# Kernel optimization log

Measured on AMD Instinct MI355X. Metric: run time of the kernel, lower is better.

Reference implementation:

```python
import jax, jax.numpy as jnp
import numpy as np

B, T = 2, 2048
D_MODEL, D_HIDDEN = 1024, 2048
N_EXPERTS, TOP_K = 8, 2
N_TOKENS = B * T
CAPACITY = 2 * N_TOKENS * TOP_K // N_EXPERTS  # 4096


def setup_inputs() -> dict:
    key = jax.random.key(0)
    k_x, k_rw, k_w, k_v, k_o = jax.random.split(key, 5)
    x = jax.random.normal(k_x, (B, T, D_MODEL), jnp.float32)
    # router: nn.Linear(d_model, n_experts) -> weight [E, D], bias [E]
    router_w = jax.random.normal(k_rw, (N_EXPERTS, D_MODEL), jnp.float32) * D_MODEL ** -0.5
    router_b = jnp.zeros((N_EXPERTS,), jnp.float32)
    # stacked expert params, matching SwiGLU init scales
    W = jax.random.normal(k_w, (N_EXPERTS, D_MODEL, D_HIDDEN), jnp.float32) * D_MODEL ** -0.5
    V = jax.random.normal(k_v, (N_EXPERTS, D_MODEL, D_HIDDEN), jnp.float32) * D_MODEL ** -0.5
    W_out = jax.random.normal(k_o, (N_EXPERTS, D_HIDDEN, D_MODEL), jnp.float32) * D_HIDDEN ** -0.5
    return {"x": x, "router_w": router_w, "router_b": router_b, "W": W, "V": V, "W_out": W_out}


def reference(x, router_w, router_b, W, V, W_out):
    Bq, Tq, D = x.shape
    N = Bq * Tq
    x_flat = x.reshape(N, D)

    # token-level top-k routing
    router_logits = x_flat @ router_w.T + router_b            # [N, E]
    top_vals, top_ids = jax.lax.top_k(router_logits, TOP_K)   # [N, K]
    top_probs = jax.nn.softmax(top_vals, axis=-1)             # [N, K]

    # pad row N: gathers with fill index N read zeros / contribute zero weight
    x_pad = jnp.concatenate([x_flat, jnp.zeros((1, D), x_flat.dtype)], axis=0)
    probs_pad = jnp.concatenate([top_probs, jnp.zeros((1, TOP_K), top_probs.dtype)], axis=0)

    out = jnp.zeros((N + 1, D), x_flat.dtype)
    for e in range(N_EXPERTS):  # static small loop over experts
        tok, slot = jnp.nonzero(top_ids == e, size=CAPACITY, fill_value=(N, 0))
        w = probs_pad[tok, slot][:, None]     # [C, 1], zero for padding slots
        xin = x_pad[tok]                      # [C, D] gather
        a = xin @ W[e]                        # [C, H]
        b = xin @ V[e]                        # [C, H]
        y = (a * (b * jax.nn.sigmoid(b))) @ W_out[e]  # SwiGLU: a * swish(b) -> [C, D]
        out = out.at[tok].add(y * w)          # weighted scatter-add
    return out[:N].reshape(Bq, Tq, D)
```

## Files before the change

### kernel.cpp

```cpp
#include <hip/hip_runtime.h>
#include <cstdint>
#include <cstddef>

#define N_TOK 4096
#define DM    1024
#define DH    2048
#define NE    8
#define NSLOT 8192

typedef short bf16x8_t __attribute__((ext_vector_type(8)));
typedef float f32x4    __attribute__((ext_vector_type(4)));
typedef unsigned short u16x8 __attribute__((ext_vector_type(8)));

__device__ __forceinline__ unsigned short f2bf(float f) {
  union { float f; unsigned int u; } v; v.f = f;
  unsigned int u = v.u;
  u += 0x7fffu + ((u >> 16) & 1u);
  return (unsigned short)(u >> 16);
}

__device__ __forceinline__ float bf2f(unsigned short h) {
  union { unsigned int u; float f; } v; v.u = ((unsigned int)h) << 16;
  return v.f;
}

#define GLD16(gp, lp)                                                          \
  __builtin_amdgcn_global_load_lds(                                            \
      (const __attribute__((address_space(1))) void*)(gp),                     \
      (__attribute__((address_space(3))) void*)(lp), 16, 0, 0)

__device__ __forceinline__ int expert_off(const int* __restrict__ counts, int e, int* cnt) {
  int off = 0, s = 0;
#pragma unroll
  for (int i = 0; i < NE; i++) { if (i == e) off = s; s += counts[i]; }
  *cnt = counts[e];
  return off;
}

__global__ __launch_bounds__(256) void k_transpose(
    const float* __restrict__ W, const float* __restrict__ V,
    const float* __restrict__ Wout, unsigned short* __restrict__ B1t,
    unsigned short* __restrict__ B2t, int* __restrict__ counts) {
  if (blockIdx.z == 0 && blockIdx.x == 0 && blockIdx.y == 0 && threadIdx.x < NE)
    counts[threadIdx.x] = 0;

  const int z = blockIdx.z;
  const float* s;
  unsigned short* d;
  int R, C, xt, yt;
  if (z < 16) {
    const int e = z & 7;
    s = ((z < 8) ? W : V) + (size_t)e * DM * DH;
    d = B1t + (size_t)e * 4096 * DM + (size_t)((z < 8) ? 0 : DH) * DM;
    R = DM; C = DH; xt = blockIdx.x; yt = blockIdx.y;
  } else {
    const int e = z - 16;
    s = Wout + (size_t)e * DH * DM;
    d = B2t + (size_t)e * DM * DH;
    R = DH; C = DM;
    const int flat = blockIdx.x * 16 + blockIdx.y;
    xt = flat & 15; yt = flat >> 4;
  }
  const int c0 = xt * 64, r0 = yt * 64;
  __shared__ float tile[64][65];
  const int t = threadIdx.x;
  {
    const int cc = (t & 15) * 4;
#pragma unroll
    for (int j = 0; j < 4; j++) {
      const int r = (t >> 4) + j * 16;
      const float4 v = *(const float4*)(s + (size_t)(r0 + r) * C + c0 + cc);
      tile[r][cc + 0] = v.x; tile[r][cc + 1] = v.y;
      tile[r][cc + 2] = v.z; tile[r][cc + 3] = v.w;
    }
  }
  __syncthreads();
  {
    const int r8 = (t & 7) * 8;
#pragma unroll
    for (int j = 0; j < 2; j++) {
      const int c = (t >> 3) + j * 32;
      u16x8 o;
#pragma unroll
      for (int i = 0; i < 8; i++) o[i] = f2bf(tile[r8 + i][c]);
      *(u16x8*)(d + (size_t)(c0 + c) * R + r0 + r8) = o;
    }
  }
}

__global__ __launch_bounds__(256) void k_router(
    const float* __restrict__ x, const float* __restrict__ rw,
    const float* __restrict__ rb, int* __restrict__ counts,
    int* __restrict__ meta_e, int* __restrict__ meta_idx,
    float* __restrict__ meta_p) {
  const int wv = threadIdx.x >> 6;
  const int l  = threadIdx.x & 63;
  const int tk = blockIdx.x * 4 + wv;
  const float* xr = x + (size_t)tk * DM;

  float acc[NE];
#pragma unroll
  for (int e = 0; e < NE; e++) acc[e] = 0.f;
#pragma unroll 4
  for (int i = 0; i < DM / 64; i++) {
    const float xv = xr[i * 64 + l];
#pragma unroll
    for (int e = 0; e < NE; e++) acc[e] += xv * rw[e * DM + i * 64 + l];
  }
#pragma unroll
  for (int off = 32; off > 0; off >>= 1) {
#pragma unroll
    for (int e = 0; e < NE; e++) acc[e] += __shfl_xor(acc[e], off);
  }
#pragma unroll
  for (int e = 0; e < NE; e++) acc[e] += rb[e];

  float v0 = -1e30f; int e0 = 0;
#pragma unroll
  for (int e = 0; e < NE; e++) { if (acc[e] > v0) { v0 = acc[e]; e0 = e; } }
  float v1 = -1e30f; int e1 = 0;
#pragma unroll
  for (int e = 0; e < NE; e++) { if (e != e0 && acc[e] > v1) { v1 = acc[e]; e1 = e; } }
  const float p0 = 1.0f / (1.0f + __expf(v1 - v0));
  const float p1 = 1.0f - p0;

  if (l == 0) {
    const int i0 = atomicAdd(&counts[e0], 1);
    const int i1 = atomicAdd(&counts[e1], 1);
    meta_e[tk * 2 + 0] = e0;  meta_e[tk * 2 + 1] = e1;
    meta_idx[tk * 2 + 0] = i0; meta_idx[tk * 2 + 1] = i1;
    meta_p[tk * 2 + 0] = p0;  meta_p[tk * 2 + 1] = p1;
  }
}

__global__ __launch_bounds__(256) void k_gather(
    const float* __restrict__ x, const int* __restrict__ meta_e,
    const int* __restrict__ meta_idx, const int* __restrict__ counts,
    unsigned short* __restrict__ Xg) {
  const int tk = blockIdx.x;
  int offs[NE];
  { int s = 0;
#pragma unroll
    for (int e = 0; e < NE; e++) { offs[e] = s; s += counts[e]; } }
  const int s0 = tk * 2, s1 = s0 + 1;
  const int g0 = offs[meta_e[s0]] + meta_idx[s0];
  const int g1 = offs[meta_e[s1]] + meta_idx[s1];
  const float4 v = ((const float4*)(x + (size_t)tk * DM))[threadIdx.x];
  ushort4 o;
  o.x = f2bf(v.x); o.y = f2bf(v.y); o.z = f2bf(v.z); o.w = f2bf(v.w);
  *(ushort4*)(Xg + (size_t)g0 * DM + threadIdx.x * 4) = o;
  *(ushort4*)(Xg + (size_t)g1 * DM + threadIdx.x * 4) = o;
}

__global__ __launch_bounds__(256, 2) void k_gemm1(
    const unsigned short* __restrict__ Xg, const unsigned short* __restrict__ B1t,
    unsigned short* __restrict__ G, const int* __restrict__ counts) {
  const int e = blockIdx.z;
  int cnt;
  const int off = expert_off(counts, e, &cnt);
  const int mt = blockIdx.y;
  if (mt * 128 >= cnt) return;
  const int h0 = blockIdx.x * 128;
  const int row_base = off + mt * 128;

  __shared__ unsigned short As[2][128 * 32];
  __shared__ unsigned short Ws[2][128 * 32];
  __shared__ unsigned short Vs[2][128 * 32];

  const int t = threadIdx.x;
  const int l = t & 63;
  const int w = t >> 6;
  const int wm = (w >> 1) * 64;
  const int wn = (w & 1) * 64;
  const int lr = l & 15;
  const int kq = (l >> 4) * 8;

  const unsigned short* Bw = B1t + ((size_t)e * 4096 + h0) * DM;
  const unsigned short* Bv = Bw + (size_t)DH * DM;

  const int c0 = t, c1 = t + 256;
  const int ar0 = c0 >> 2, ak0 = (c0 & 3) * 8;
  const int ar1 = c1 >> 2, ak1 = (c1 & 3) * 8;
  const int arow0 = min(row_base + ar0, NSLOT - 1);
  const int arow1 = min(row_base + ar1, NSLOT - 1);

  f32x4 acc_a[4][4], acc_b[4][4];
  const f32x4 z4 = {0.f, 0.f, 0.f, 0.f};
#pragma unroll
  for (int i = 0; i < 4; i++)
#pragma unroll
    for (int j = 0; j < 4; j++) { acc_a[i][j] = z4; acc_b[i][j] = z4; }

  for (int k0 = 0; k0 < DM; k0 += 64) {
    __syncthreads();
    GLD16(Xg + (size_t)arow0 * DM + k0 + ak0,      &As[0][c0 * 8]);
    GLD16(Xg + (size_t)arow1 * DM + k0 + ak1,      &As[0][c1 * 8]);
    GLD16(Xg + (size_t)arow0 * DM + k0 + 32 + ak0, &As[1][c0 * 8]);
    GLD16(Xg + (size_t)arow1 * DM + k0 + 32 + ak1, &As[1][c1 * 8]);
    GLD16(Bw + (size_t)ar0 * DM + k0 + ak0,        &Ws[0][c0 * 8]);
    GLD16(Bw + (size_t)ar1 * DM + k0 + ak1,        &Ws[0][c1 * 8]);
    GLD16(Bw + (size_t)ar0 * DM + k0 + 32 + ak0,   &Ws[1][c0 * 8]);
    GLD16(Bw + (size_t)ar1 * DM + k0 + 32 + ak1,   &Ws[1][c1 * 8]);
    GLD16(Bv + (size_t)ar0 * DM + k0 + ak0,        &Vs[0][c0 * 8]);
    GLD16(Bv + (size_t)ar1 * DM + k0 + ak1,        &Vs[0][c1 * 8]);
    GLD16(Bv + (size_t)ar0 * DM + k0 + 32 + ak0,   &Vs[1][c0 * 8]);
    GLD16(Bv + (size_t)ar1 * DM + k0 + 32 + ak1,   &Vs[1][c1 * 8]);
    __syncthreads();

#pragma unroll
    for (int ks = 0; ks < 2; ks++) {
      bf16x8_t af[4], wf[4], vf[4];
#pragma unroll
      for (int mi = 0; mi < 4; mi++)
        af[mi] = *(const bf16x8_t*)&As[ks][(wm + mi * 16 + lr) * 32 + kq];
#pragma unroll
      for (int ni = 0; ni < 4; ni++) {
        wf[ni] = *(const bf16x8_t*)&Ws[ks][(wn + ni * 16 + lr) * 32 + kq];
        vf[ni] = *(const bf16x8_t*)&Vs[ks][(wn + ni * 16 + lr) * 32 + kq];
      }
#pragma unroll
      for (int mi = 0; mi < 4; mi++)
#pragma unroll
        for (int ni = 0; ni < 4; ni++) {
          acc_a[mi][ni] = __builtin_amdgcn_mfma_f32_16x16x32_bf16(af[mi], wf[ni], acc_a[mi][ni], 0, 0, 0);
          acc_b[mi][ni] = __builtin_amdgcn_mfma_f32_16x16x32_bf16(af[mi], vf[ni], acc_b[mi][ni], 0, 0, 0);
        }
    }
  }

  const int q4 = (l >> 4) * 4;
#pragma unroll
  for (int mi = 0; mi < 4; mi++) {
#pragma unroll
    for (int r = 0; r < 4; r++) {
      const int mloc = mt * 128 + wm + mi * 16 + q4 + r;
      if (mloc >= cnt) continue;
      unsigned short* grow = G + (size_t)(off + mloc) * DH;
#pragma unroll
      for (int ni = 0; ni < 4; ni++) {
        const int h = h0 + wn + ni * 16 + lr;
        const float a = acc_a[mi][ni][r];
        const float b = acc_b[mi][ni][r];
        const float s = b / (1.0f + __expf(-b));
        grow[h] = f2bf(a * s);
      }
    }
  }
}

__global__ __launch_bounds__(256, 2) void k_gemm2(
    const unsigned short* __restrict__ G, const unsigned short* __restrict__ B2t,
    unsigned short* __restrict__ Y, const int* __restrict__ counts) {
  const int z = blockIdx.z;
  const int e = z & 7;
  const int half = z >> 3;
  int cnt;
  const int off = expert_off(counts, e, &cnt);
  const int mt = blockIdx.y;
  if (mt * 128 >= cnt) return;
  const int n0 = blockIdx.x * 128;
  const int row_base = off + mt * 128;
  const int kbase = half * 1024;

  __shared__ unsigned short As[2][128 * 32];
  __shared__ unsigned short Bs[2][128 * 32];

  const int t = threadIdx.x;
  const int l = t & 63;
  const int w = t >> 6;
  const int wm = (w >> 1) * 64;
  const int wn = (w & 1) * 64;
  const int lr = l & 15;
  const int kq = (l >> 4) * 8;

  const unsigned short* Bp = B2t + ((size_t)e * DM + n0) * DH;

  const int c0 = t, c1 = t + 256;
  const int ar0 = c0 >> 2, ak0 = (c0 & 3) * 8;
  const int ar1 = c1 >> 2, ak1 = (c1 & 3) * 8;
  const int arow0 = min(row_base + ar0, NSLOT - 1);
  const int arow1 = min(row_base + ar1, NSLOT - 1);

  f32x4 acc[4][4];
  const f32x4 z4 = {0.f, 0.f, 0.f, 0.f};
#pragma unroll
  for (int i = 0; i < 4; i++)
#pragma unroll
    for (int j = 0; j < 4; j++) acc[i][j] = z4;

  for (int kk = 0; kk < 1024; kk += 64) {
    const int k0 = kbase + kk;
    __syncthreads();
    GLD16(G + (size_t)arow0 * DH + k0 + ak0,      &As[0][c0 * 8]);
    GLD16(G + (size_t)arow1 * DH + k0 + ak1,      &As[0][c1 * 8]);
    GLD16(G + (size_t)arow0 * DH + k0 + 32 + ak0, &As[1][c0 * 8]);
    GLD16(G + (size_t)arow1 * DH + k0 + 32 + ak1, &As[1][c1 * 8]);
    GLD16(Bp + (size_t)ar0 * DH + k0 + ak0,       &Bs[0][c0 * 8]);
    GLD16(Bp + (size_t)ar1 * DH + k0 + ak1,       &Bs[0][c1 * 8]);
    GLD16(Bp + (size_t)ar0 * DH + k0 + 32 + ak0,  &Bs[1][c0 * 8]);
    GLD16(Bp + (size_t)ar1 * DH + k0 + 32 + ak1,  &Bs[1][c1 * 8]);
    __syncthreads();

#pragma unroll
    for (int ks = 0; ks < 2; ks++) {
      bf16x8_t af[4], bf[4];
#pragma unroll
      for (int mi = 0; mi < 4; mi++)
        af[mi] = *(const bf16x8_t*)&As[ks][(wm + mi * 16 + lr) * 32 + kq];
#pragma unroll
      for (int ni = 0; ni < 4; ni++)
        bf[ni] = *(const bf16x8_t*)&Bs[ks][(wn + ni * 16 + lr) * 32 + kq];
#pragma unroll
      for (int mi = 0; mi < 4; mi++)
#pragma unroll
        for (int ni = 0; ni < 4; ni++)
          acc[mi][ni] = __builtin_amdgcn_mfma_f32_16x16x32_bf16(af[mi], bf[ni], acc[mi][ni], 0, 0, 0);
    }
  }

  unsigned short* Yh = Y + (size_t)half * NSLOT * DM;
  const int q4 = (l >> 4) * 4;
#pragma unroll
  for (int mi = 0; mi < 4; mi++) {
#pragma unroll
    for (int r = 0; r < 4; r++) {
      const int mloc = mt * 128 + wm + mi * 16 + q4 + r;
      if (mloc >= cnt) continue;
      unsigned short* yrow = Yh + (size_t)(off + mloc) * DM;
#pragma unroll
      for (int ni = 0; ni < 4; ni++)
        yrow[n0 + wn + ni * 16 + lr] = f2bf(acc[mi][ni][r]);
    }
  }
}

__global__ __launch_bounds__(256) void k_combine(
    const unsigned short* __restrict__ Y, const int* __restrict__ meta_e,
    const int* __restrict__ meta_idx, const float* __restrict__ meta_p,
    const int* __restrict__ counts, float* __restrict__ out) {
  const int tk = blockIdx.x;
  int offs[NE];
  { int s = 0;
#pragma unroll
    for (int e = 0; e < NE; e++) { offs[e] = s; s += counts[e]; } }
  const int s0 = tk * 2, s1 = s0 + 1;
  const int g0 = offs[meta_e[s0]] + meta_idx[s0];
  const int g1 = offs[meta_e[s1]] + meta_idx[s1];
  const float w0 = meta_p[s0], w1 = meta_p[s1];
  const unsigned short* Y1 = Y + (size_t)NSLOT * DM;
  const ushort4 a0 = ((const ushort4*)(Y  + (size_t)g0 * DM))[threadIdx.x];
  const ushort4 a1 = ((const ushort4*)(Y1 + (size_t)g0 * DM))[threadIdx.x];
  const ushort4 b0 = ((const ushort4*)(Y  + (size_t)g1 * DM))[threadIdx.x];
  const ushort4 b1 = ((const ushort4*)(Y1 + (size_t)g1 * DM))[threadIdx.x];
  float4 o;
  o.x = w0 * (bf2f(a0.x) + bf2f(a1.x)) + w1 * (bf2f(b0.x) + bf2f(b1.x));
  o.y = w0 * (bf2f(a0.y) + bf2f(a1.y)) + w1 * (bf2f(b0.y) + bf2f(b1.y));
  o.z = w0 * (bf2f(a0.z) + bf2f(a1.z)) + w1 * (bf2f(b0.z) + bf2f(b1.z));
  o.w = w0 * (bf2f(a0.w) + bf2f(a1.w)) + w1 * (bf2f(b0.w) + bf2f(b1.w));
  ((float4*)(out + (size_t)tk * DM))[threadIdx.x] = o;
}

extern "C" void kernel_launch(void* const* d_in, const int* in_sizes, int n_in,
                              void* d_out, int out_size, void* d_ws, size_t ws_size,
                              hipStream_t stream) {
  const float* x    = (const float*)d_in[0];
  const float* rw   = (const float*)d_in[1];
  const float* rb   = (const float*)d_in[2];
  const float* W    = (const float*)d_in[3];
  const float* V    = (const float*)d_in[4];
  const float* Wout = (const float*)d_in[5];
  float* out = (float*)d_out;

  char* p = (char*)d_ws;
  unsigned short* B1t = (unsigned short*)p; p += (size_t)NE * 4096 * DM * 2;
  unsigned short* Y   = (unsigned short*)B1t;
  unsigned short* B2t = (unsigned short*)p; p += (size_t)NE * DM * DH * 2;
  unsigned short* Xg  = (unsigned short*)p; p += (size_t)NSLOT * DM * 2;
  unsigned short* G   = (unsigned short*)p; p += (size_t)NSLOT * DH * 2;
  int*   counts      = (int*)p;   p += 256;
  int*   meta_e      = (int*)p;   p += (size_t)N_TOK * 2 * 4;
  int*   meta_idx    = (int*)p;   p += (size_t)N_TOK * 2 * 4;
  float* meta_p      = (float*)p; p += (size_t)N_TOK * 2 * 4;

  k_transpose<<<dim3(32, 16, 24), 256, 0, stream>>>(W, V, Wout, B1t, B2t, counts);
  k_router<<<N_TOK / 4, 256, 0, stream>>>(x, rw, rb, counts, meta_e, meta_idx, meta_p);
  k_gather<<<N_TOK, 256, 0, stream>>>(x, meta_e, meta_idx, counts, Xg);
  k_gemm1<<<dim3(DH / 128, NSLOT / 128, NE), 256, 0, stream>>>(Xg, B1t, G, counts);
  k_gemm2<<<dim3(DM / 128, NSLOT / 128, 2 * NE), 256, 0, stream>>>(G, B2t, Y, counts);
  k_combine<<<N_TOK, 256, 0, stream>>>(Y, meta_e, meta_idx, meta_p, counts, out);
}
```

Measured before the change: 493.1 us.

## Pipeline expert GEMMs with 4-stage async LDS buffers, swizzle, 256-row tiles

Both expert GEMM kernels move to 512-thread blocks with 256-row M tiles and a 4-deep ring of LDS stages filled by global_load_lds. Loads for stage s+3 are issued before computing stage s, with explicit vmcnt waits and a single barrier per step instead of two full syncs per K chunk. An XOR swizzle is applied to the LDS layout to cut bank conflicts on fragment reads, and MFMA sections run at raised wave priority. LDS use grows considerably (about 160KB for gemm1), which may limit occupancy to one block per CU despite the launch bound, and larger M tiles waste more work on partially filled expert tiles.

```diff
diff --git a/kernel.cpp b/kernel.cpp
--- a/kernel.cpp
+++ b/kernel.cpp
@@ -28,6 +28,14 @@
   __builtin_amdgcn_global_load_lds(                                            \
       (const __attribute__((address_space(1))) void*)(gp),                     \
       (__attribute__((address_space(3))) void*)(lp), 16, 0, 0)
+
+#define WAITVM(N) asm volatile("s_waitcnt vmcnt(" #N ")" ::: "memory")
+#define BAR()                                                                  \
+  do {                                                                         \
+    __builtin_amdgcn_sched_barrier(0);                                         \
+    __builtin_amdgcn_s_barrier();                                              \
+    __builtin_amdgcn_sched_barrier(0);                                         \
+  } while (0)
 
 __device__ __forceinline__ int expert_off(const int* __restrict__ counts, int e, int* cnt) {
   int off = 0, s = 0;
@@ -152,20 +160,20 @@
   *(ushort4*)(Xg + (size_t)g1 * DM + threadIdx.x * 4) = o;
 }
 
-__global__ __launch_bounds__(256, 2) void k_gemm1(
+__global__ __launch_bounds__(512, 2) void k_gemm1(
     const unsigned short* __restrict__ Xg, const unsigned short* __restrict__ B1t,
     unsigned short* __restrict__ G, const int* __restrict__ counts) {
   const int e = blockIdx.z;
   int cnt;
   const int off = expert_off(counts, e, &cnt);
   const int mt = blockIdx.y;
-  if (mt * 128 >= cnt) return;
+  if (mt * 256 >= cnt) return;
   const int h0 = blockIdx.x * 128;
-  const int row_base = off + mt * 128;
-
-  __shared__ unsigned short As[2][128 * 32];
-  __shared__ unsigned short Ws[2][128 * 32];
-  __shared__ unsigned short Vs[2][128 * 32];
+  const int row_base = off + mt * 256;
+
+  __shared__ unsigned short As[4][256 * 32];
+  __shared__ unsigned short Ws[4][128 * 32];
+  __shared__ unsigned short Vs[4][128 * 32];
 
   const int t = threadIdx.x;
   const int l = t & 63;
@@ -178,11 +186,27 @@
   const unsigned short* Bw = B1t + ((size_t)e * 4096 + h0) * DM;
   const unsigned short* Bv = Bw + (size_t)DH * DM;
 
-  const int c0 = t, c1 = t + 256;
-  const int ar0 = c0 >> 2, ak0 = (c0 & 3) * 8;
-  const int ar1 = c1 >> 2, ak1 = (c1 & 3) * 8;
-  const int arow0 = min(row_base + ar0, NSLOT - 1);
-  const int arow1 = min(row_base + ar1, NSLOT - 1);
+  const int cA0 = t, cA1 = t + 512;
+  const int rA0 = cA0 >> 2, rA1 = cA1 >> 2;
+  const int kA0 = ((cA0 & 3) ^ ((rA0 >> 1) & 3)) << 3;
+  const int kA1 = ((cA1 & 3) ^ ((rA1 >> 1) & 3)) << 3;
+  const size_t aoff0 = (size_t)min(row_base + rA0, NSLOT - 1) * DM + kA0;
+  const size_t aoff1 = (size_t)min(row_base + rA1, NSLOT - 1) * DM + kA1;
+  const int rB = t >> 2;
+  const int kB = ((t & 3) ^ ((rB >> 1) & 3)) << 3;
+  const size_t boff = (size_t)rB * DM + kB;
+
+#define STAGE1(s)                                                              \
+  do {                                                                         \
+    const int k0_ = (s) * 32;                                                  \
+    unsigned short* As_ = As[(s) & 3];                                         \
+    unsigned short* Ws_ = Ws[(s) & 3];                                         \
+    unsigned short* Vs_ = Vs[(s) & 3];                                         \
+    GLD16(Xg + aoff0 + k0_, &As_[cA0 * 8]);                                    \
+    GLD16(Xg + aoff1 + k0_, &As_[cA1 * 8]);                                    \
+    GLD16(Bw + boff + k0_, &Ws_[t * 8]);                                       \
+    GLD16(Bv + boff + k0_, &Vs_[t * 8]);                                       \
+  } while (0)
 
   f32x4 acc_a[4][4], acc_b[4][4];
   const f32x4 z4 = {0.f, 0.f, 0.f, 0.f};
@@ -191,49 +215,52 @@
 #pragma unroll
     for (int j = 0; j < 4; j++) { acc_a[i][j] = z4; acc_b[i][j] = z4; }
 
-  for (int k0 = 0; k0 < DM; k0 += 64) {
-    __syncthreads();
-    GLD16(Xg + (size_t)arow0 * DM + k0 + ak0,      &As[0][c0 * 8]);
-    GLD16(Xg + (size_t)arow1 * DM + k0 + ak1,      &As[0][c1 * 8]);
-    GLD16(Xg + (size_t)arow0 * DM + k0 + 32 + ak0, &As[1][c0 * 8]);
-    GLD16(Xg + (size_t)arow1 * DM + k0 + 32 + ak1, &As[1][c1 * 8]);
-    GLD16(Bw + (size_t)ar0 * DM + k0 + ak0,        &Ws[0][c0 * 8]);
-    GLD16(Bw + (size_t)ar1 * DM + k0 + ak1,        &Ws[0][c1 * 8]);
-    GLD16(Bw + (size_t)ar0 * DM + k0 + 32 + ak0,   &Ws[1][c0 * 8]);
-    GLD16(Bw + (size_t)ar1 * DM + k0 + 32 + ak1,   &Ws[1][c1 * 8]);
-    GLD16(Bv + (size_t)ar0 * DM + k0 + ak0,        &Vs[0][c0 * 8]);
-    GLD16(Bv + (size_t)ar1 * DM + k0 + ak1,        &Vs[0][c1 * 8]);
-    GLD16(Bv + (size_t)ar0 * DM + k0 + 32 + ak0,   &Vs[1][c0 * 8]);
-    GLD16(Bv + (size_t)ar1 * DM + k0 + 32 + ak1,   &Vs[1][c1 * 8]);
-    __syncthreads();
-
-#pragma unroll
-    for (int ks = 0; ks < 2; ks++) {
-      bf16x8_t af[4], wf[4], vf[4];
-#pragma unroll
-      for (int mi = 0; mi < 4; mi++)
-        af[mi] = *(const bf16x8_t*)&As[ks][(wm + mi * 16 + lr) * 32 + kq];
+  STAGE1(0); STAGE1(1); STAGE1(2);
+  WAITVM(8);
+  BAR();
+
+  const int NS = DM / 32;
+#pragma unroll 2
+  for (int s = 0; s < NS; s++) {
+    if (s + 3 < NS) STAGE1(s + 3);
+    const unsigned short* Asl = As[s & 3];
+    const unsigned short* Wsl = Ws[s & 3];
+    const unsigned short* Vsl = Vs[s & 3];
+    bf16x8_t af[4], wf[4], vf[4];
+#pragma unroll
+    for (int mi = 0; mi < 4; mi++) {
+      const int row = wm + mi * 16 + lr;
+      af[mi] = *(const bf16x8_t*)&Asl[(row * 32 + kq) ^ (((row >> 1) & 3) << 3)];
+    }
+#pragma unroll
+    for (int ni = 0; ni < 4; ni++) {
+      const int row = wn + ni * 16 + lr;
+      const int idx = (row * 32 + kq) ^ (((row >> 1) & 3) << 3);
+      wf[ni] = *(const bf16x8_t*)&Wsl[idx];
+      vf[ni] = *(const bf16x8_t*)&Vsl[idx];
+    }
+    __builtin_amdgcn_s_setprio(1);
+#pragma unroll
+    for (int mi = 0; mi < 4; mi++)
 #pragma unroll
       for (int ni = 0; ni < 4; ni++) {
-        wf[ni] = *(const bf16x8_t*)&Ws[ks][(wn + ni * 16 + lr) * 32 + kq];
-        vf[ni] = *(const bf16x8_t*)&Vs[ks][(wn + ni * 16 + lr) * 32 + kq];
+        acc_a[mi][ni] = __builtin_amdgcn_mfma_f32_16x16x32_bf16(af[mi], wf[ni], acc_a[mi][ni], 0, 0, 0);
+        acc_b[mi][ni] = __builtin_amdgcn_mfma_f32_16x16x32_bf16(af[mi], vf[ni], acc_b[mi][ni], 0, 0, 0);
       }
-#pragma unroll
-      for (int mi = 0; mi < 4; mi++)
-#pragma unroll
-        for (int ni = 0; ni < 4; ni++) {
-          acc_a[mi][ni] = __builtin_amdgcn_mfma_f32_16x16x32_bf16(af[mi], wf[ni], acc_a[mi][ni], 0, 0, 0);
-          acc_b[mi][ni] = __builtin_amdgcn_mfma_f32_16x16x32_bf16(af[mi], vf[ni], acc_b[mi][ni], 0, 0, 0);
-        }
-    }
-  }
+    __builtin_amdgcn_s_setprio(0);
+    if (s < NS - 3)       { WAITVM(8); }
+    else if (s == NS - 3) { WAITVM(4); }
+    else if (s == NS - 2) { WAITVM(0); }
+    if (s < NS - 1) BAR();
+  }
+#undef STAGE1
 
   const int q4 = (l >> 4) * 4;
 #pragma unroll
   for (int mi = 0; mi < 4; mi++) {
 #pragma unroll
     for (int r = 0; r < 4; r++) {
-      const int mloc = mt * 128 + wm + mi * 16 + q4 + r;
+      const int mloc = mt * 256 + wm + mi * 16 + q4 + r;
       if (mloc >= cnt) continue;
       unsigned short* grow = G + (size_t)(off + mloc) * DH;
 #pragma unroll
@@ -241,14 +268,14 @@
         const int h = h0 + wn + ni * 16 + lr;
         const float a = acc_a[mi][ni][r];
         const float b = acc_b[mi][ni][r];
-        const float s = b / (1.0f + __expf(-b));
-        grow[h] = f2bf(a * s);
+        const float sgl = b / (1.0f + __expf(-b));
+        grow[h] = f2bf(a * sgl);
       }
     }
   }
 }
 
-__global__ __launch_bounds__(256, 2) void k_gemm2(
+__global__ __launch_bounds__(512, 2) void k_gemm2(
     const unsigned short* __restrict__ G, const unsigned short* __restrict__ B2t,
     unsigned short* __restrict__ Y, const int* __restrict__ counts) {
   const int z = blockIdx.z;
@@ -257,13 +284,13 @@
   int cnt;
   const int off = expert_off(counts, e, &cnt);
   const int mt = blockIdx.y;
-  if (mt * 128 >= cnt) return;
+  if (mt * 256 >= cnt) return;
   const int n0 = blockIdx.x * 128;
-  const int row_base = off + mt * 128;
+  const int row_base = off + mt * 256;
   const int kbase = half * 1024;
 
-  __shared__ unsigned short As[2][128 * 32];
-  __shared__ unsigned short Bs[2][128 * 32];
+  __shared__ unsigned short As[4][256 * 32];
+  __shared__ unsigned short Bs[4][128 * 32];
 
   const int t = threadIdx.x;
   const int l = t & 63;
@@ -275,11 +302,25 @@
 
   const unsigned short* Bp = B2t + ((size_t)e * DM + n0) * DH;
 
-  const int c0 = t, c1 = t + 256;
-  const int ar0 = c0 >> 2, ak0 = (c0 & 3) * 8;
-  const int ar1 = c1 >> 2, ak1 = (c1 & 3) * 8;
-  const int arow0 = min(row_base + ar0, NSLOT - 1);
-  const int arow1 = min(row_base + ar1, NSLOT - 1);
+  const int cA0 = t, cA1 = t + 512;
+  const int rA0 = cA0 >> 2, rA1 = cA1 >> 2;
+  const int kA0 = ((cA0 & 3) ^ ((rA0 >> 1) & 3)) << 3;
+  const int kA1 = ((cA1 & 3) ^ ((rA1 >> 1) & 3)) << 3;
+  const size_t aoff0 = (size_t)min(row_base + rA0, NSLOT - 1) * DH + kA0;
+  const size_t aoff1 = (size_t)min(row_base + rA1, NSLOT - 1) * DH + kA1;
+  const int rB = t >> 2;
+  const int kB = ((t & 3) ^ ((rB >> 1) & 3)) << 3;
+  const size_t boff = (size_t)rB * DH + kB;
+
+#define STAGE2(s)                                                              \
+  do {                                                                         \
+    const int k0_ = kbase + (s) * 32;                                          \
+    unsigned short* As_ = As[(s) & 3];                                         \
+    unsigned short* Bs_ = Bs[(s) & 3];                                         \
+    GLD16(G + aoff0 + k0_, &As_[cA0 * 8]);                                     \
+    GLD16(G + aoff1 + k0_, &As_[cA1 * 8]);                                     \
+    GLD16(Bp + boff + k0_, &Bs_[t * 8]);                                       \
+  } while (0)
 
   f32x4 acc[4][4];
   const f32x4 z4 = {0.f, 0.f, 0.f, 0.f};
@@ -288,35 +329,40 @@
 #pragma unroll
     for (int j = 0; j < 4; j++) acc[i][j] = z4;
 
-  for (int kk = 0; kk < 1024; kk += 64) {
-    const int k0 = kbase + kk;
-    __syncthreads();
-    GLD16(G + (size_t)arow0 * DH + k0 + ak0,      &As[0][c0 * 8]);
-    GLD16(G + (size_t)arow1 * DH + k0 + ak1,      &As[0][c1 * 8]);
-    GLD16(G + (size_t)arow0 * DH + k0 + 32 + ak0, &As[1][c0 * 8]);
-    GLD16(G + (size_t)arow1 * DH + k0 + 32 + ak1, &As[1][c1 * 8]);
-    GLD16(Bp + (size_t)ar0 * DH + k0 + ak0,       &Bs[0][c0 * 8]);
-    GLD16(Bp + (size_t)ar1 * DH + k0 + ak1,       &Bs[0][c1 * 8]);
-    GLD16(Bp + (size_t)ar0 * DH + k0 + 32 + ak0,  &Bs[1][c0 * 8]);
-    GLD16(Bp + (size_t)ar1 * DH + k0 + 32 + ak1,  &Bs[1][c1 * 8]);
-    __syncthreads();
-
-#pragma unroll
-    for (int ks = 0; ks < 2; ks++) {
-      bf16x8_t af[4], bf[4];
-#pragma unroll
-      for (int mi = 0; mi < 4; mi++)
-        af[mi] = *(const bf16x8_t*)&As[ks][(wm + mi * 16 + lr) * 32 + kq];
+  STAGE2(0); STAGE2(1); STAGE2(2);
+  WAITVM(6);
+  BAR();
+
+  const int NS = 1024 / 32;
+#pragma unroll 2
+  for (int s = 0; s < NS; s++) {
+    if (s + 3 < NS) STAGE2(s + 3);
+    const unsigned short* Asl = As[s & 3];
+    const unsigned short* Bsl = Bs[s & 3];
+    bf16x8_t af[4], bf[4];
+#pragma unroll
+    for (int mi = 0; mi < 4; mi++) {
+      const int row = wm + mi * 16 + lr;
+      af[mi] = *(const bf16x8_t*)&Asl[(row * 32 + kq) ^ (((row >> 1) & 3) << 3)];
+    }
+#pragma unroll
+    for (int ni = 0; ni < 4; ni++) {
+      const int row = wn + ni * 16 + lr;
+      bf[ni] = *(const bf16x8_t*)&Bsl[(row * 32 + kq) ^ (((row >> 1) & 3) << 3)];
+    }
+    __builtin_amdgcn_s_setprio(1);
+#pragma unroll
+    for (int mi = 0; mi < 4; mi++)
 #pragma unroll
       for (int ni = 0; ni < 4; ni++)
-        bf[ni] = *(const bf16x8_t*)&Bs[ks][(wn + ni * 16 + lr) * 32 + kq];
-#pragma unroll
-      for (int mi = 0; mi < 4; mi++)
-#pragma unroll
-        for (int ni = 0; ni < 4; ni++)
-          acc[mi][ni] = __builtin_amdgcn_mfma_f32_16x16x32_bf16(af[mi], bf[ni], acc[mi][ni], 0, 0, 0);
-    }
-  }
+        acc[mi][ni] = __builtin_amdgcn_mfma_f32_16x16x32_bf16(af[mi], bf[ni], acc[mi][ni], 0, 0, 0);
+    __builtin_amdgcn_s_setprio(0);
+    if (s < NS - 3)       { WAITVM(6); }
+    else if (s == NS - 3) { WAITVM(3); }
+    else if (s == NS - 2) { WAITVM(0); }
+    if (s < NS - 1) BAR();
+  }
+#undef STAGE2
 
   unsigned short* Yh = Y + (size_t)half * NSLOT * DM;
   const int q4 = (l >> 4) * 4;
@@ -324,7 +370,7 @@
   for (int mi = 0; mi < 4; mi++) {
 #pragma unroll
     for (int r = 0; r < 4; r++) {
-      const int mloc = mt * 128 + wm + mi * 16 + q4 + r;
+      const int mloc = mt * 256 + wm + mi * 16 + q4 + r;
       if (mloc >= cnt) continue;
       unsigned short* yrow = Yh + (size_t)(off + mloc) * DM;
 #pragma unroll
@@ -385,7 +431,7 @@
   k_transpose<<<dim3(32, 16, 24), 256, 0, stream>>>(W, V, Wout, B1t, B2t, counts);
   k_router<<<N_TOK / 4, 256, 0, stream>>>(x, rw, rb, counts, meta_e, meta_idx, meta_p);
   k_gather<<<N_TOK, 256, 0, stream>>>(x, meta_e, meta_idx, counts, Xg);
-  k_gemm1<<<dim3(DH / 128, NSLOT / 128, NE), 256, 0, stream>>>(Xg, B1t, G, counts);
-  k_gemm2<<<dim3(DM / 128, NSLOT / 128, 2 * NE), 256, 0, stream>>>(G, B2t, Y, counts);
+  k_gemm1<<<dim3(DH / 128, NSLOT / 256, NE), 512, 0, stream>>>(Xg, B1t, G, counts);
+  k_gemm2<<<dim3(DM / 128, NSLOT / 256, 2 * NE), 512, 0, stream>>>(G, B2t, Y, counts);
   k_combine<<<N_TOK, 256, 0, stream>>>(Y, meta_e, meta_idx, meta_p, counts, out);
 }
```

New measurement: 549.0 us. 11.3% more time.

## Double-buffer LDS tiles with prefetch and XOR-swizzle layout in both expert GEMMs

Applied to the files above, without the earlier changes.

Both grouped GEMM kernels now stage 32-wide K slices into two alternating LDS buffers, issuing the next slice's global-to-LDS loads before the MFMA work on the current slice. This replaces the old load-all-then-compute structure with its two barriers per 64-wide step. The K offset inside each 32-element row is also XOR-swizzled by row bits, applied consistently on store and read, to cut LDS bank conflicts on fragment reads. The cost is one barrier per 32-K step instead of per 64-K step, and it relies on GLD16 being asynchronous enough to overlap with compute.

```diff
diff --git a/kernel.cpp b/kernel.cpp
--- a/kernel.cpp
+++ b/kernel.cpp
@@ -179,10 +179,23 @@
   const unsigned short* Bv = Bw + (size_t)DH * DM;
 
   const int c0 = t, c1 = t + 256;
-  const int ar0 = c0 >> 2, ak0 = (c0 & 3) * 8;
-  const int ar1 = c1 >> 2, ak1 = (c1 & 3) * 8;
-  const int arow0 = min(row_base + ar0, NSLOT - 1);
-  const int arow1 = min(row_base + ar1, NSLOT - 1);
+  const int r0 = c0 >> 2, r1 = c1 >> 2;
+  const int k0s = ((c0 & 3) ^ ((r0 >> 1) & 3)) << 3;
+  const int k1s = ((c1 & 3) ^ ((r1 >> 1) & 3)) << 3;
+  const size_t aoff0 = (size_t)min(row_base + r0, NSLOT - 1) * DM + k0s;
+  const size_t aoff1 = (size_t)min(row_base + r1, NSLOT - 1) * DM + k1s;
+  const size_t boff0 = (size_t)r0 * DM + k0s;
+  const size_t boff1 = (size_t)r1 * DM + k1s;
+
+#define STG1(buf, kk)                                                          \
+  do {                                                                         \
+    GLD16(Xg + aoff0 + (kk), &As[buf][c0 * 8]);                                \
+    GLD16(Xg + aoff1 + (kk), &As[buf][c1 * 8]);                                \
+    GLD16(Bw + boff0 + (kk), &Ws[buf][c0 * 8]);                                \
+    GLD16(Bw + boff1 + (kk), &Ws[buf][c1 * 8]);                                \
+    GLD16(Bv + boff0 + (kk), &Vs[buf][c0 * 8]);                                \
+    GLD16(Bv + boff1 + (kk), &Vs[buf][c1 * 8]);                                \
+  } while (0)
 
   f32x4 acc_a[4][4], acc_b[4][4];
   const f32x4 z4 = {0.f, 0.f, 0.f, 0.f};
@@ -191,42 +204,36 @@
 #pragma unroll
     for (int j = 0; j < 4; j++) { acc_a[i][j] = z4; acc_b[i][j] = z4; }
 
-  for (int k0 = 0; k0 < DM; k0 += 64) {
+  STG1(0, 0);
+  __syncthreads();
+
+  const int NS = DM / 32;
+  for (int s = 0; s < NS; s++) {
+    const int cur = s & 1;
+    bf16x8_t af[4], wf[4], vf[4];
+#pragma unroll
+    for (int mi = 0; mi < 4; mi++) {
+      const int row = wm + mi * 16 + lr;
+      af[mi] = *(const bf16x8_t*)&As[cur][(row * 32 + kq) ^ (((row >> 1) & 3) << 3)];
+    }
+#pragma unroll
+    for (int ni = 0; ni < 4; ni++) {
+      const int row = wn + ni * 16 + lr;
+      const int idx = (row * 32 + kq) ^ (((row >> 1) & 3) << 3);
+      wf[ni] = *(const bf16x8_t*)&Ws[cur][idx];
+      vf[ni] = *(const bf16x8_t*)&Vs[cur][idx];
+    }
+    if (s + 1 < NS) STG1(cur ^ 1, (s + 1) * 32);
+#pragma unroll
+    for (int mi = 0; mi < 4; mi++)
+#pragma unroll
+      for (int ni = 0; ni < 4; ni++) {
+        acc_a[mi][ni] = __builtin_amdgcn_mfma_f32_16x16x32_bf16(af[mi], wf[ni], acc_a[mi][ni], 0, 0, 0);
+        acc_b[mi][ni] = __builtin_amdgcn_mfma_f32_16x16x32_bf16(af[mi], vf[ni], acc_b[mi][ni], 0, 0, 0);
+      }
     __syncthreads();
-    GLD16(Xg + (size_t)arow0 * DM + k0 + ak0,      &As[0][c0 * 8]);
-    GLD16(Xg + (size_t)arow1 * DM + k0 + ak1,      &As[0][c1 * 8]);
-    GLD16(Xg + (size_t)arow0 * DM + k0 + 32 + ak0, &As[1][c0 * 8]);
-    GLD16(Xg + (size_t)arow1 * DM + k0 + 32 + ak1, &As[1][c1 * 8]);
-    GLD16(Bw + (size_t)ar0 * DM + k0 + ak0,        &Ws[0][c0 * 8]);
-    GLD16(Bw + (size_t)ar1 * DM + k0 + ak1,        &Ws[0][c1 * 8]);
-    GLD16(Bw + (size_t)ar0 * DM + k0 + 32 + ak0,   &Ws[1][c0 * 8]);
-    GLD16(Bw + (size_t)ar1 * DM + k0 + 32 + ak1,   &Ws[1][c1 * 8]);
-    GLD16(Bv + (size_t)ar0 * DM + k0 + ak0,        &Vs[0][c0 * 8]);
-    GLD16(Bv + (size_t)ar1 * DM + k0 + ak1,        &Vs[0][c1 * 8]);
-    GLD16(Bv + (size_t)ar0 * DM + k0 + 32 + ak0,   &Vs[1][c0 * 8]);
-    GLD16(Bv + (size_t)ar1 * DM + k0 + 32 + ak1,   &Vs[1][c1 * 8]);
-    __syncthreads();
-
-#pragma unroll
-    for (int ks = 0; ks < 2; ks++) {
-      bf16x8_t af[4], wf[4], vf[4];
-#pragma unroll
-      for (int mi = 0; mi < 4; mi++)
-        af[mi] = *(const bf16x8_t*)&As[ks][(wm + mi * 16 + lr) * 32 + kq];
-#pragma unroll
-      for (int ni = 0; ni < 4; ni++) {
-        wf[ni] = *(const bf16x8_t*)&Ws[ks][(wn + ni * 16 + lr) * 32 + kq];
-        vf[ni] = *(const bf16x8_t*)&Vs[ks][(wn + ni * 16 + lr) * 32 + kq];
-      }
-#pragma unroll
-      for (int mi = 0; mi < 4; mi++)
-#pragma unroll
-        for (int ni = 0; ni < 4; ni++) {
-          acc_a[mi][ni] = __builtin_amdgcn_mfma_f32_16x16x32_bf16(af[mi], wf[ni], acc_a[mi][ni], 0, 0, 0);
-          acc_b[mi][ni] = __builtin_amdgcn_mfma_f32_16x16x32_bf16(af[mi], vf[ni], acc_b[mi][ni], 0, 0, 0);
-        }
-    }
-  }
+  }
+#undef STG1
 
   const int q4 = (l >> 4) * 4;
 #pragma unroll
@@ -241,8 +248,8 @@
         const int h = h0 + wn + ni * 16 + lr;
         const float a = acc_a[mi][ni][r];
         const float b = acc_b[mi][ni][r];
-        const float s = b / (1.0f + __expf(-b));
-        grow[h] = f2bf(a * s);
+        const float sgl = b / (1.0f + __expf(-b));
+        grow[h] = f2bf(a * sgl);
       }
     }
   }
@@ -276,10 +283,21 @@
   const unsigned short* Bp = B2t + ((size_t)e * DM + n0) * DH;
 
   const int c0 = t, c1 = t + 256;
-  const int ar0 = c0 >> 2, ak0 = (c0 & 3) * 8;
-  const int ar1 = c1 >> 2, ak1 = (c1 & 3) * 8;
-  const int arow0 = min(row_base + ar0, NSLOT - 1);
-  const int arow1 = min(row_base + ar1, NSLOT - 1);
+  const int r0 = c0 >> 2, r1 = c1 >> 2;
+  const int k0s = ((c0 & 3) ^ ((r0 >> 1) & 3)) << 3;
+  const int k1s = ((c1 & 3) ^ ((r1 >> 1) & 3)) << 3;
+  const size_t aoff0 = (size_t)min(row_base + r0, NSLOT - 1) * DH + k0s;
+  const size_t aoff1 = (size_t)min(row_base + r1, NSLOT - 1) * DH + k1s;
+  const size_t boff0 = (size_t)r0 * DH + k0s;
+  const size_t boff1 = (size_t)r1 * DH + k1s;
+
+#define STG2(buf, kk)                                                          \
+  do {                                                                         \
+    GLD16(G + aoff0 + (kk), &As[buf][c0 * 8]);                                 \
+    GLD16(G + aoff1 + (kk), &As[buf][c1 * 8]);                                 \
+    GLD16(Bp + boff0 + (kk), &Bs[buf][c0 * 8]);                                \
+    GLD16(Bp + boff1 + (kk), &Bs[buf][c1 * 8]);                                \
+  } while (0)
 
   f32x4 acc[4][4];
   const f32x4 z4 = {0.f, 0.f, 0.f, 0.f};
@@ -288,35 +306,32 @@
 #pragma unroll
     for (int j = 0; j < 4; j++) acc[i][j] = z4;
 
-  for (int kk = 0; kk < 1024; kk += 64) {
-    const int k0 = kbase + kk;
+  STG2(0, kbase);
+  __syncthreads();
+
+  const int NS = 1024 / 32;
+  for (int s = 0; s < NS; s++) {
+    const int cur = s & 1;
+    bf16x8_t af[4], bf[4];
+#pragma unroll
+    for (int mi = 0; mi < 4; mi++) {
+      const int row = wm + mi * 16 + lr;
+      af[mi] = *(const bf16x8_t*)&As[cur][(row * 32 + kq) ^ (((row >> 1) & 3) << 3)];
+    }
+#pragma unroll
+    for (int ni = 0; ni < 4; ni++) {
+      const int row = wn + ni * 16 + lr;
+      bf[ni] = *(const bf16x8_t*)&Bs[cur][(row * 32 + kq) ^ (((row >> 1) & 3) << 3)];
+    }
+    if (s + 1 < NS) STG2(cur ^ 1, kbase + (s + 1) * 32);
+#pragma unroll
+    for (int mi = 0; mi < 4; mi++)
+#pragma unroll
+      for (int ni = 0; ni < 4; ni++)
+        acc[mi][ni] = __builtin_amdgcn_mfma_f32_16x16x32_bf16(af[mi], bf[ni], acc[mi][ni], 0, 0, 0);
     __syncthreads();
-    GLD16(G + (size_t)arow0 * DH + k0 + ak0,      &As[0][c0 * 8]);
-    GLD16(G + (size_t)arow1 * DH + k0 + ak1,      &As[0][c1 * 8]);
-    GLD16(G + (size_t)arow0 * DH + k0 + 32 + ak0, &As[1][c0 * 8]);
-    GLD16(G + (size_t)arow1 * DH + k0 + 32 + ak1, &As[1][c1 * 8]);
-    GLD16(Bp + (size_t)ar0 * DH + k0 + ak0,       &Bs[0][c0 * 8]);
-    GLD16(Bp + (size_t)ar1 * DH + k0 + ak1,       &Bs[0][c1 * 8]);
-    GLD16(Bp + (size_t)ar0 * DH + k0 + 32 + ak0,  &Bs[1][c0 * 8]);
-    GLD16(Bp + (size_t)ar1 * DH + k0 + 32 + ak1,  &Bs[1][c1 * 8]);
-    __syncthreads();
-
-#pragma unroll
-    for (int ks = 0; ks < 2; ks++) {
-      bf16x8_t af[4], bf[4];
-#pragma unroll
-      for (int mi = 0; mi < 4; mi++)
-        af[mi] = *(const bf16x8_t*)&As[ks][(wm + mi * 16 + lr) * 32 + kq];
-#pragma unroll
-      for (int ni = 0; ni < 4; ni++)
-        bf[ni] = *(const bf16x8_t*)&Bs[ks][(wn + ni * 16 + lr) * 32 + kq];
-#pragma unroll
-      for (int mi = 0; mi < 4; mi++)
-#pragma unroll
-        for (int ni = 0; ni < 4; ni++)
-          acc[mi][ni] = __builtin_amdgcn_mfma_f32_16x16x32_bf16(af[mi], bf[ni], acc[mi][ni], 0, 0, 0);
-    }
-  }
+  }
+#undef STG2
 
   unsigned short* Yh = Y + (size_t)half * NSLOT * DM;
   const int q4 = (l >> 4) * 4;
```

New measurement: 501.6 us. No clear change (+1.7%).
